# Optimization experiments

Hardware: AMD Instinct MI355X
Metric: run time of the kernel (lower is better)

## Reference

```python
import jax, jax.numpy as jnp
import numpy as np

B, S, D = 16, 2048, 512

def setup_inputs() -> dict:
    key = jax.random.key(0)
    k0, k1, k2, k3 = jax.random.split(key, 4)
    scale = 1.0 / np.sqrt(D)
    return {
        "inputs": jax.random.normal(k0, (B, S, D), dtype=jnp.float32),
        "W_q": jax.random.normal(k1, (D, D), dtype=jnp.float32) * scale,
        "W_k": jax.random.normal(k2, (D, D), dtype=jnp.float32) * scale,
        "W_v": jax.random.normal(k3, (D, D), dtype=jnp.float32) * scale,
    }

def reference(inputs, W_q, W_k, W_v):
    # Q/K/V projections: [B,S,D]
    q = jnp.einsum('bsd,de->bse', inputs, W_q)
    k = jnp.einsum('bsd,de->bse', inputs, W_k)
    v = jnp.einsum('bsd,de->bse', inputs, W_v)
    d_k = jnp.asarray(q.shape[-1], dtype=q.dtype)
    scores = jnp.einsum('bqd,bkd->bqk', q, k) / jnp.sqrt(d_k)  # [B,S,S]
    attn = jax.nn.softmax(scores, axis=-1)
    out = jnp.einsum('bqk,bkd->bqd', attn, v)  # [B,S,D]
    return jnp.sum(out, axis=1)  # sum-pool over seq -> [B,D]
```

## Files before the change

kernel.cpp:

```cpp
#include <hip/hip_runtime.h>
#include <hip/hip_bf16.h>


#define S_LEN 2048
#define D_DIM 512
#define BATCH 16

typedef short bf16x8 __attribute__((ext_vector_type(8)));
typedef float f32x4 __attribute__((ext_vector_type(4)));

typedef __attribute__((address_space(3))) void lds_void_t;
typedef const __attribute__((address_space(1))) void gbl_void_t;

__device__ __forceinline__ void async_copy16(const void* g, void* l) {
  __builtin_amdgcn_global_load_lds((gbl_void_t*)g, (lds_void_t*)l, 16, 0, 0);
}

__device__ __forceinline__ unsigned short f2bf(float f) {
  unsigned u = __float_as_uint(f);
  u += 0x7fff + ((u >> 16) & 1);
  return (unsigned short)(u >> 16);
}
__device__ __forceinline__ float bf2f(unsigned short h) {
  return __uint_as_float((unsigned)h << 16);
}

__device__ __forceinline__ unsigned enc8(float x) {
  unsigned u = __float_as_uint(x);
  unsigned t = (u + 0x7FFFFu + ((u >> 20) & 1u)) >> 20;
  int b = (int)t - 0x3C0;
  b = b < 0 ? 0 : (b > 127 ? 127 : b);
  return (unsigned)b;
}
__device__ __forceinline__ float dec8(unsigned b) {
  return b ? __uint_as_float((b + 0x3C0u) << 20) : 0.0f;
}

__device__ __forceinline__ void gemm_core_nt(
    const unsigned short* __restrict__ A, long lda,
    const unsigned short* __restrict__ B, long ldb,
    int K, unsigned short* As, unsigned short* Bs, f32x4 acc[4][4])
{
  const int tid  = threadIdx.x;
  const int lane = tid & 63;
  const int w    = tid >> 6;
  const int wm   = w >> 1, wn = w & 1;
  const int r16  = lane & 15;
  const int kq   = lane >> 4;

  const int j0 = w * 64 + lane;
  const int j1 = (w + 4) * 64 + lane;
  const int r0 = j0 >> 2, cc0 = (((j0 & 3) - (r0 >> 1)) & 3);
  const int r1 = j1 >> 2, cc1 = (((j1 & 3) - (r1 >> 1)) & 3);

  const long a0 = (long)r0 * lda + cc0 * 8;
  const long a1 = (long)r1 * lda + cc1 * 8;
  const long b0 = (long)r0 * ldb + cc0 * 8;
  const long b1 = (long)r1 * ldb + cc1 * 8;

  int aoff[4], boff[4];
#pragma unroll
  for (int mt = 0; mt < 4; ++mt) {
    const int row = wm * 64 + mt * 16 + r16;
    aoff[mt] = row * 32 + (((row >> 1) + kq) & 3) * 8;
  }
#pragma unroll
  for (int nt = 0; nt < 4; ++nt) {
    const int row = wn * 64 + nt * 16 + r16;
    boff[nt] = row * 32 + (((row >> 1) + kq) & 3) * 8;
  }

  for (int k0 = 0; k0 < K; k0 += 32) {
    __syncthreads();
    async_copy16(A + a0 + k0, (char*)As + (w    ) * 1024);
    async_copy16(A + a1 + k0, (char*)As + (w + 4) * 1024);
    async_copy16(B + b0 + k0, (char*)Bs + (w    ) * 1024);
    async_copy16(B + b1 + k0, (char*)Bs + (w + 4) * 1024);
    __syncthreads();

    bf16x8 af[4], bg[4];
#pragma unroll
    for (int mt = 0; mt < 4; ++mt) af[mt] = *(const bf16x8*)&As[aoff[mt]];
#pragma unroll
    for (int nt = 0; nt < 4; ++nt) bg[nt] = *(const bf16x8*)&Bs[boff[nt]];
#pragma unroll
    for (int mt = 0; mt < 4; ++mt)
#pragma unroll
      for (int nt = 0; nt < 4; ++nt)
        acc[mt][nt] = __builtin_amdgcn_mfma_f32_16x16x32_bf16(af[mt], bg[nt], acc[mt][nt], 0, 0, 0);
  }
}

__global__ __launch_bounds__(256) void k_zero(float* __restrict__ p, int n) {
  int i = blockIdx.x * 256 + threadIdx.x;
  if (i < n) p[i] = 0.0f;
}

__global__ __launch_bounds__(256) void k_cast(const float* __restrict__ s, unsigned short* __restrict__ d) {
  int i = (blockIdx.x * 256 + threadIdx.x) * 4;
  float4 v = *(const float4*)(s + i);
  ushort4 o;
  o.x = f2bf(v.x); o.y = f2bf(v.y); o.z = f2bf(v.z); o.w = f2bf(v.w);
  *(ushort4*)(d + i) = o;
}

__global__ __launch_bounds__(256) void k_castW(
    const float* __restrict__ a, const float* __restrict__ b,
    unsigned short* __restrict__ da, unsigned short* __restrict__ db)
{
  const int blk = blockIdx.x;
  const float* s = (blk < 256) ? a : b;
  unsigned short* d = (blk < 256) ? da : db;
  int i = ((blk & 255) * 256 + threadIdx.x) * 4;
  float4 v = *(const float4*)(s + i);
  ushort4 o;
  o.x = f2bf(v.x); o.y = f2bf(v.y); o.z = f2bf(v.z); o.w = f2bf(v.w);
  *(ushort4*)(d + i) = o;
}

__global__ __launch_bounds__(256) void k_gemm_bf16out(
    const unsigned short* __restrict__ A, long lda,
    const unsigned short* __restrict__ B, long ldb, int K,
    unsigned short* __restrict__ C, long ldc, float scale)
{
  __shared__ alignas(16) unsigned short As[128 * 32];
  __shared__ alignas(16) unsigned short Bs[128 * 32];
  f32x4 acc[4][4] = {};
  const long am0 = (long)blockIdx.y * 128;
  const long bn0 = (long)blockIdx.x * 128;
  gemm_core_nt(A + am0 * lda, lda, B + bn0 * ldb, ldb, K, As, Bs, acc);

  const int lane = threadIdx.x & 63;
  const int w = threadIdx.x >> 6, wm = w >> 1, wn = w & 1;
  const long row0 = am0 + wm * 64 + (lane >> 4) * 4;
  const long col0 = bn0 + wn * 64 + (lane & 15);
#pragma unroll
  for (int mt = 0; mt < 4; ++mt)
#pragma unroll
    for (int nt = 0; nt < 4; ++nt)
#pragma unroll
      for (int r = 0; r < 4; ++r)
        C[(row0 + mt * 16 + r) * ldc + col0 + nt * 16] = f2bf(acc[mt][nt][r] * scale);
}

union SMemAE {
  struct { unsigned short As[128 * 32]; unsigned short Bs[128 * 32]; } s;
  unsigned E32[128 * 36];
};

__global__ __launch_bounds__(256) void k_passAE(
    const unsigned short* __restrict__ Ybf, const unsigned short* __restrict__ Xbf,
    float* __restrict__ lrow, unsigned* __restrict__ E)
{
  __shared__ SMemAE sm;
  f32x4 acc[4][4] = {};
  const int b = blockIdx.z, qt = blockIdx.y, kt = blockIdx.x;
  const long q0 = (long)qt * 128;
  const long n0 = (long)kt * 128;
  gemm_core_nt(Ybf + ((long)b * S_LEN + q0) * D_DIM, D_DIM,
               Xbf + ((long)b * S_LEN + n0) * D_DIM, D_DIM, D_DIM,
               sm.s.As, sm.s.Bs, acc);

  const int lane = threadIdx.x & 63;
  const int w = threadIdx.x >> 6, wm = w >> 1, wn = w & 1;
  const int r16 = lane & 15, quad = lane >> 4;

  __syncthreads();

#pragma unroll
  for (int mt = 0; mt < 4; ++mt) {
    float rs[4] = {0.f, 0.f, 0.f, 0.f};
#pragma unroll
    for (int nt = 0; nt < 4; ++nt) {
      unsigned dw = 0;
#pragma unroll
      for (int r = 0; r < 4; ++r) {
        float e = __builtin_amdgcn_exp2f(acc[mt][nt][r]);
        rs[r] += e;
        dw |= enc8(e) << (8 * r);
      }
      const int col = wn * 64 + nt * 16 + r16;
      const int r4  = wm * 16 + mt * 4 + quad;
      sm.E32[col * 36 + r4] = dw;
    }
#pragma unroll
    for (int r = 0; r < 4; ++r) {
      float s = rs[r];
      s += __shfl_xor(s, 1, 64);
      s += __shfl_xor(s, 2, 64);
      s += __shfl_xor(s, 4, 64);
      s += __shfl_xor(s, 8, 64);
      if (r16 == 0)
        atomicAdd(&lrow[(long)b * S_LEN + q0 + wm * 64 + mt * 16 + quad * 4 + r], s);
    }
  }
  __syncthreads();

  unsigned* Eg = E + (((long)(b * 16 + qt)) * 16 + kt) * 4096;
  const int t = threadIdx.x;
#pragma unroll
  for (int p = 0; p < 4; ++p) {
    const int n = p * 256 + t;
    const int col = n >> 3, hj = n & 7;
    uint4 v = *(const uint4*)&sm.E32[col * 36 + hj * 4];
    *(uint4*)(Eg + n * 4) = v;
  }
}

__global__ __launch_bounds__(256) void k_wsum(
    const unsigned* __restrict__ E, const float* __restrict__ lrow,
    float* __restrict__ wcol)
{
  __shared__ float rl[512];
  const int kt = blockIdx.x, qq = blockIdx.y, b = blockIdx.z;
  const int tid = threadIdx.x;
  {
    const float* lp = lrow + (long)b * S_LEN + qq * 512;
    rl[tid]       = 1.0f / lp[tid];
    rl[tid + 256] = 1.0f / lp[tid + 256];
  }
  __syncthreads();
  const int col = tid & 127, qsel = tid >> 7;
  float acc = 0.0f;
#pragma unroll
  for (int qt2 = 0; qt2 < 2; ++qt2) {
    const int qtl = qsel * 2 + qt2;
    const int qt = qq * 4 + qtl;
    const unsigned* Ep = E + (((long)(b * 16 + qt)) * 16 + kt) * 4096 + col * 32;
    const float* rlq = rl + qtl * 128;
#pragma unroll
    for (int j = 0; j < 8; ++j) {
      uint4 v = *(const uint4*)(Ep + j * 4);
      const unsigned dws[4] = {v.x, v.y, v.z, v.w};
#pragma unroll
      for (int i = 0; i < 4; ++i) {
        const unsigned dv = dws[i];
        const float* r = rlq + j * 16 + i * 4;
        acc += dec8( dv        & 0xFFu) * r[0];
        acc += dec8((dv >>  8) & 0xFFu) * r[1];
        acc += dec8((dv >> 16) & 0xFFu) * r[2];
        acc += dec8((dv >> 24)        ) * r[3];
      }
    }
  }
  atomicAdd(&wcol[(long)b * S_LEN + kt * 128 + col], acc);
}

__global__ __launch_bounds__(256) void k_passA(
    const unsigned short* __restrict__ Ybf, const unsigned short* __restrict__ Xbf,
    float* __restrict__ lrow)
{
  __shared__ alignas(16) unsigned short As[128 * 32];
  __shared__ alignas(16) unsigned short Bs[128 * 32];
  f32x4 acc[4][4] = {};
  const int b = blockIdx.z;
  const long q0 = (long)blockIdx.y * 128;
  const long n0 = (long)blockIdx.x * 128;
  gemm_core_nt(Ybf + ((long)b * S_LEN + q0) * D_DIM, D_DIM,
               Xbf + ((long)b * S_LEN + n0) * D_DIM, D_DIM, D_DIM, As, Bs, acc);

  const int lane = threadIdx.x & 63;
  const int w = threadIdx.x >> 6, wm = w >> 1;
#pragma unroll
  for (int mt = 0; mt < 4; ++mt) {
#pragma unroll
    for (int r = 0; r < 4; ++r) {
      float s = 0.0f;
#pragma unroll
      for (int nt = 0; nt < 4; ++nt) s += __builtin_amdgcn_exp2f(acc[mt][nt][r]);
      s += __shfl_xor(s, 1, 64);
      s += __shfl_xor(s, 2, 64);
      s += __shfl_xor(s, 4, 64);
      s += __shfl_xor(s, 8, 64);
      if ((lane & 15) == 0)
        atomicAdd(&lrow[(long)b * S_LEN + q0 + wm * 64 + mt * 16 + (lane >> 4) * 4 + r], s);
    }
  }
}

__global__ __launch_bounds__(256) void k_passB(
    const unsigned short* __restrict__ Ybf, const unsigned short* __restrict__ Xbf,
    const float* __restrict__ lrow, float* __restrict__ wcol)
{
  __shared__ alignas(16) unsigned short As[128 * 32];
  __shared__ alignas(16) unsigned short Bs[128 * 32];
  f32x4 acc[4][4] = {};
  const int b = blockIdx.z;
  const long q0 = (long)blockIdx.y * 128;
  const long n0 = (long)blockIdx.x * 128;
  gemm_core_nt(Ybf + ((long)b * S_LEN + q0) * D_DIM, D_DIM,
               Xbf + ((long)b * S_LEN + n0) * D_DIM, D_DIM, D_DIM, As, Bs, acc);

  const int lane = threadIdx.x & 63;
  const int w = threadIdx.x >> 6, wm = w >> 1, wn = w & 1;
  float csv[4] = {0.0f, 0.0f, 0.0f, 0.0f};
#pragma unroll
  for (int mt = 0; mt < 4; ++mt) {
    const float4 lv = *(const float4*)&lrow[(long)b * S_LEN + q0 + wm * 64 + mt * 16 + (lane >> 4) * 4];
    const float rv[4] = {1.0f / lv.x, 1.0f / lv.y, 1.0f / lv.z, 1.0f / lv.w};
#pragma unroll
    for (int nt = 0; nt < 4; ++nt)
#pragma unroll
      for (int r = 0; r < 4; ++r)
        csv[nt] += __builtin_amdgcn_exp2f(acc[mt][nt][r]) * rv[r];
  }
#pragma unroll
  for (int nt = 0; nt < 4; ++nt) {
    csv[nt] += __shfl_xor(csv[nt], 16, 64);
    csv[nt] += __shfl_xor(csv[nt], 32, 64);
  }
  if (lane < 16) {
#pragma unroll
    for (int nt = 0; nt < 4; ++nt)
      atomicAdd(&wcol[(long)b * S_LEN + n0 + wn * 64 + nt * 16 + lane], csv[nt]);
  }
}

__global__ __launch_bounds__(256) void k_t(
    const unsigned short* __restrict__ Xbf, const float* __restrict__ wcol,
    float* __restrict__ tvec)
{
  const int b = blockIdx.z;
  const int d = blockIdx.x * 256 + threadIdx.x;
  const int k0 = blockIdx.y * 256;
  const unsigned short* Xp = Xbf + ((long)b * S_LEN + k0) * D_DIM + d;
  const float* wp = wcol + (long)b * S_LEN + k0;
  float acc = 0.0f;
#pragma unroll 4
  for (int k = 0; k < 256; ++k) acc += wp[k] * bf2f(Xp[(long)k * D_DIM]);
  atomicAdd(&tvec[b * D_DIM + d], acc);
}

__global__ __launch_bounds__(128) void k_out(
    const float* __restrict__ tvec, const float* __restrict__ Wv, float* __restrict__ out)
{
  __shared__ float tl[512];
  const int b = blockIdx.y;
  const int e = blockIdx.x * 128 + threadIdx.x;
#pragma unroll
  for (int j = 0; j < 4; ++j) tl[threadIdx.x + j * 128] = tvec[b * D_DIM + threadIdx.x + j * 128];
  __syncthreads();
  float acc = 0.0f;
#pragma unroll 4
  for (int d = 0; d < 512; ++d) acc += tl[d] * Wv[(long)d * D_DIM + e];
  out[b * D_DIM + e] = acc;
}

extern "C" void kernel_launch(void* const* d_in, const int* in_sizes, int n_in,
                              void* d_out, int out_size, void* d_ws, size_t ws_size,
                              hipStream_t stream) {
  const float* X  = (const float*)d_in[0];
  const float* Wq = (const float*)d_in[1];
  const float* Wk = (const float*)d_in[2];
  const float* Wv = (const float*)d_in[3];
  float* out = (float*)d_out;

  char* ws = (char*)d_ws;
  unsigned short* Xbf = (unsigned short*)(ws);
  unsigned short* Ybf = (unsigned short*)(ws + 33554432);
  unsigned short* Mt  = (unsigned short*)(ws + 67108864);
  unsigned short* Wqb = (unsigned short*)(ws + 67633152);
  unsigned short* Wkb = (unsigned short*)(ws + 68157440);
  float* lrow = (float*)(ws + 68681728);
  float* wcol = (float*)(ws + 68812800);
  float* tvec = (float*)(ws + 68943872);
  unsigned* E = (unsigned*)(ws + 69206016);
  const bool bigws = ws_size >= (size_t)69206016 + (size_t)67108864;

  k_zero<<<288, 256, 0, stream>>>(lrow, 73728);

  k_cast<<<16384, 256, 0, stream>>>(X, Xbf);
  k_castW<<<512, 256, 0, stream>>>(Wq, Wk, Wqb, Wkb);

  const float scale = 1.4426950408889634f / 22.627416997969522f;
  k_gemm_bf16out<<<dim3(4, 4), 256, 0, stream>>>(Wkb, 512, Wqb, 512, 512, Mt, 512, scale);

  k_gemm_bf16out<<<dim3(4, 256), 256, 0, stream>>>(Xbf, 512, Mt, 512, 512, Ybf, 512, 1.0f);

  if (bigws) {
    k_passAE<<<dim3(16, 16, 16), 256, 0, stream>>>(Ybf, Xbf, lrow, E);
    k_wsum<<<dim3(16, 4, 16), 256, 0, stream>>>(E, lrow, wcol);
  } else {
    k_passA<<<dim3(16, 16, 16), 256, 0, stream>>>(Ybf, Xbf, lrow);
    k_passB<<<dim3(16, 16, 16), 256, 0, stream>>>(Ybf, Xbf, lrow, wcol);
  }

  k_t<<<dim3(2, 8, 16), 256, 0, stream>>>(Xbf, wcol, tvec);
  k_out<<<dim3(4, 16), 128, 0, stream>>>(tvec, Wv, out);
}
```

Measured before the change: 324.1 us.

## Widen GEMM K-tile to 64, use hardware FP8 encode, split tail kernels

```diff
diff --git a/kernel.cpp b/kernel.cpp
--- a/kernel.cpp
+++ b/kernel.cpp
@@ -24,6 +24,12 @@
 __device__ __forceinline__ float bf2f(unsigned short h) {
   return __uint_as_float((unsigned)h << 16);
 }
+
+#if __has_builtin(__builtin_amdgcn_cvt_pk_fp8_f32) && __has_builtin(__builtin_amdgcn_cvt_f32_fp8)
+#define HAVE_FP8CVT 1
+#else
+#define HAVE_FP8CVT 0
+#endif
 
 __device__ __forceinline__ unsigned enc8(float x) {
   unsigned u = __float_as_uint(x);
@@ -36,6 +42,16 @@
   return b ? __uint_as_float((b + 0x3C0u) << 20) : 0.0f;
 }
 
+__device__ __forceinline__ unsigned pack4_fp8(float e0, float e1, float e2, float e3) {
+#if HAVE_FP8CVT
+  unsigned dw = (unsigned)__builtin_amdgcn_cvt_pk_fp8_f32(e0, e1, 0, false);
+  dw = (unsigned)__builtin_amdgcn_cvt_pk_fp8_f32(e2, e3, (int)dw, true);
+  return dw;
+#else
+  return enc8(e0) | (enc8(e1) << 8) | (enc8(e2) << 16) | (enc8(e3) << 24);
+#endif
+}
+
 __device__ __forceinline__ void gemm_core_nt(
     const unsigned short* __restrict__ A, long lda,
     const unsigned short* __restrict__ B, long ldb,
@@ -48,52 +64,58 @@
   const int r16  = lane & 15;
   const int kq   = lane >> 4;
 
-  const int j0 = w * 64 + lane;
-  const int j1 = (w + 4) * 64 + lane;
-  const int r0 = j0 >> 2, cc0 = (((j0 & 3) - (r0 >> 1)) & 3);
-  const int r1 = j1 >> 2, cc1 = (((j1 & 3) - (r1 >> 1)) & 3);
-
-  const long a0 = (long)r0 * lda + cc0 * 8;
-  const long a1 = (long)r1 * lda + cc1 * 8;
-  const long b0 = (long)r0 * ldb + cc0 * 8;
-  const long b1 = (long)r1 * ldb + cc1 * 8;
-
-  int aoff[4], boff[4];
-#pragma unroll
-  for (int mt = 0; mt < 4; ++mt) {
-    const int row = wm * 64 + mt * 16 + r16;
-    aoff[mt] = row * 32 + (((row >> 1) + kq) & 3) * 8;
-  }
-#pragma unroll
-  for (int nt = 0; nt < 4; ++nt) {
-    const int row = wn * 64 + nt * 16 + r16;
-    boff[nt] = row * 32 + (((row >> 1) + kq) & 3) * 8;
-  }
-
-  for (int k0 = 0; k0 < K; k0 += 32) {
+  long asrc[4], bsrc[4];
+#pragma unroll
+  for (int p = 0; p < 4; ++p) {
+    const int j = p * 256 + w * 64 + lane;
+    const int r = j >> 3, s = j & 7, c = (s - r) & 7;
+    asrc[p] = (long)r * lda + c * 8;
+    bsrc[p] = (long)r * ldb + c * 8;
+  }
+
+  int aoff[2][4], boff[2][4];
+#pragma unroll
+  for (int ks = 0; ks < 2; ++ks) {
+#pragma unroll
+    for (int t = 0; t < 4; ++t) {
+      const int m = wm * 64 + t * 16 + r16;
+      aoff[ks][t] = m * 64 + ((ks * 4 + kq + m) & 7) * 8;
+      const int n = wn * 64 + t * 16 + r16;
+      boff[ks][t] = n * 64 + ((ks * 4 + kq + n) & 7) * 8;
+    }
+  }
+
+  for (int k0 = 0; k0 < K; k0 += 64) {
     __syncthreads();
-    async_copy16(A + a0 + k0, (char*)As + (w    ) * 1024);
-    async_copy16(A + a1 + k0, (char*)As + (w + 4) * 1024);
-    async_copy16(B + b0 + k0, (char*)Bs + (w    ) * 1024);
-    async_copy16(B + b1 + k0, (char*)Bs + (w + 4) * 1024);
+#pragma unroll
+    for (int p = 0; p < 4; ++p) {
+      async_copy16(A + asrc[p] + k0, (char*)As + (p * 256 + w * 64) * 16);
+      async_copy16(B + bsrc[p] + k0, (char*)Bs + (p * 256 + w * 64) * 16);
+    }
     __syncthreads();
 
-    bf16x8 af[4], bg[4];
-#pragma unroll
-    for (int mt = 0; mt < 4; ++mt) af[mt] = *(const bf16x8*)&As[aoff[mt]];
-#pragma unroll
-    for (int nt = 0; nt < 4; ++nt) bg[nt] = *(const bf16x8*)&Bs[boff[nt]];
-#pragma unroll
-    for (int mt = 0; mt < 4; ++mt)
-#pragma unroll
-      for (int nt = 0; nt < 4; ++nt)
-        acc[mt][nt] = __builtin_amdgcn_mfma_f32_16x16x32_bf16(af[mt], bg[nt], acc[mt][nt], 0, 0, 0);
-  }
-}
-
-__global__ __launch_bounds__(256) void k_zero(float* __restrict__ p, int n) {
+#pragma unroll
+    for (int ks = 0; ks < 2; ++ks) {
+      bf16x8 af[4], bg[4];
+#pragma unroll
+      for (int mt = 0; mt < 4; ++mt) af[mt] = *(const bf16x8*)&As[aoff[ks][mt]];
+#pragma unroll
+      for (int nt = 0; nt < 4; ++nt) bg[nt] = *(const bf16x8*)&Bs[boff[ks][nt]];
+#pragma unroll
+      for (int mt = 0; mt < 4; ++mt)
+#pragma unroll
+        for (int nt = 0; nt < 4; ++nt)
+          acc[mt][nt] = __builtin_amdgcn_mfma_f32_16x16x32_bf16(af[mt], bg[nt], acc[mt][nt], 0, 0, 0);
+    }
+  }
+}
+
+__global__ __launch_bounds__(256) void k_zero2(float* __restrict__ p1, int n1,
+                                               float* __restrict__ p2, int n2) {
   int i = blockIdx.x * 256 + threadIdx.x;
-  if (i < n) p[i] = 0.0f;
+  if (i < n1) p1[i] = 0.0f;
+  i -= n1;
+  if (i >= 0 && i < n2) p2[i] = 0.0f;
 }
 
 __global__ __launch_bounds__(256) void k_cast(const float* __restrict__ s, unsigned short* __restrict__ d) {
@@ -123,8 +145,8 @@
     const unsigned short* __restrict__ B, long ldb, int K,
     unsigned short* __restrict__ C, long ldc, float scale)
 {
-  __shared__ alignas(16) unsigned short As[128 * 32];
-  __shared__ alignas(16) unsigned short Bs[128 * 32];
+  __shared__ alignas(16) unsigned short As[128 * 64];
+  __shared__ alignas(16) unsigned short Bs[128 * 64];
   f32x4 acc[4][4] = {};
   const long am0 = (long)blockIdx.y * 128;
   const long bn0 = (long)blockIdx.x * 128;
@@ -143,8 +165,8 @@
         C[(row0 + mt * 16 + r) * ldc + col0 + nt * 16] = f2bf(acc[mt][nt][r] * scale);
 }
 
-union SMemAE {
-  struct { unsigned short As[128 * 32]; unsigned short Bs[128 * 32]; } s;
+union alignas(16) SMemAE {
+  struct { unsigned short As[128 * 64]; unsigned short Bs[128 * 64]; } s;
   unsigned E32[128 * 36];
 };
 
@@ -172,16 +194,15 @@
     float rs[4] = {0.f, 0.f, 0.f, 0.f};
 #pragma unroll
     for (int nt = 0; nt < 4; ++nt) {
-      unsigned dw = 0;
+      float ev[4];
 #pragma unroll
       for (int r = 0; r < 4; ++r) {
-        float e = __builtin_amdgcn_exp2f(acc[mt][nt][r]);
-        rs[r] += e;
-        dw |= enc8(e) << (8 * r);
+        ev[r] = __builtin_amdgcn_exp2f(acc[mt][nt][r]);
+        rs[r] += ev[r];
       }
       const int col = wn * 64 + nt * 16 + r16;
       const int r4  = wm * 16 + mt * 4 + quad;
-      sm.E32[col * 36 + r4] = dw;
+      sm.E32[col * 36 + r4] = pack4_fp8(ev[0], ev[1], ev[2], ev[3]);
     }
 #pragma unroll
     for (int r = 0; r < 4; ++r) {
@@ -236,10 +257,17 @@
       for (int i = 0; i < 4; ++i) {
         const unsigned dv = dws[i];
         const float* r = rlq + j * 16 + i * 4;
+#if HAVE_FP8CVT
+        acc += __builtin_amdgcn_cvt_f32_fp8((int)dv, 0) * r[0];
+        acc += __builtin_amdgcn_cvt_f32_fp8((int)dv, 1) * r[1];
+        acc += __builtin_amdgcn_cvt_f32_fp8((int)dv, 2) * r[2];
+        acc += __builtin_amdgcn_cvt_f32_fp8((int)dv, 3) * r[3];
+#else
         acc += dec8( dv        & 0xFFu) * r[0];
         acc += dec8((dv >>  8) & 0xFFu) * r[1];
         acc += dec8((dv >> 16) & 0xFFu) * r[2];
         acc += dec8((dv >> 24)        ) * r[3];
+#endif
       }
     }
   }
@@ -250,8 +278,8 @@
     const unsigned short* __restrict__ Ybf, const unsigned short* __restrict__ Xbf,
     float* __restrict__ lrow)
 {
-  __shared__ alignas(16) unsigned short As[128 * 32];
-  __shared__ alignas(16) unsigned short Bs[128 * 32];
+  __shared__ alignas(16) unsigned short As[128 * 64];
+  __shared__ alignas(16) unsigned short Bs[128 * 64];
   f32x4 acc[4][4] = {};
   const int b = blockIdx.z;
   const long q0 = (long)blockIdx.y * 128;
@@ -282,8 +310,8 @@
     const unsigned short* __restrict__ Ybf, const unsigned short* __restrict__ Xbf,
     const float* __restrict__ lrow, float* __restrict__ wcol)
 {
-  __shared__ alignas(16) unsigned short As[128 * 32];
-  __shared__ alignas(16) unsigned short Bs[128 * 32];
+  __shared__ alignas(16) unsigned short As[128 * 64];
+  __shared__ alignas(16) unsigned short Bs[128 * 64];
   f32x4 acc[4][4] = {};
   const int b = blockIdx.z;
   const long q0 = (long)blockIdx.y * 128;
@@ -322,28 +350,28 @@
 {
   const int b = blockIdx.z;
   const int d = blockIdx.x * 256 + threadIdx.x;
-  const int k0 = blockIdx.y * 256;
+  const int k0 = blockIdx.y * 64;
   const unsigned short* Xp = Xbf + ((long)b * S_LEN + k0) * D_DIM + d;
   const float* wp = wcol + (long)b * S_LEN + k0;
   float acc = 0.0f;
-#pragma unroll 4
-  for (int k = 0; k < 256; ++k) acc += wp[k] * bf2f(Xp[(long)k * D_DIM]);
+#pragma unroll 8
+  for (int k = 0; k < 64; ++k) acc += wp[k] * bf2f(Xp[(long)k * D_DIM]);
   atomicAdd(&tvec[b * D_DIM + d], acc);
 }
 
 __global__ __launch_bounds__(128) void k_out(
     const float* __restrict__ tvec, const float* __restrict__ Wv, float* __restrict__ out)
 {
-  __shared__ float tl[512];
+  __shared__ float tl[128];
   const int b = blockIdx.y;
+  const int d0 = blockIdx.z * 128;
   const int e = blockIdx.x * 128 + threadIdx.x;
-#pragma unroll
-  for (int j = 0; j < 4; ++j) tl[threadIdx.x + j * 128] = tvec[b * D_DIM + threadIdx.x + j * 128];
+  tl[threadIdx.x] = tvec[b * D_DIM + d0 + threadIdx.x];
   __syncthreads();
   float acc = 0.0f;
-#pragma unroll 4
-  for (int d = 0; d < 512; ++d) acc += tl[d] * Wv[(long)d * D_DIM + e];
-  out[b * D_DIM + e] = acc;
+#pragma unroll 8
+  for (int d = 0; d < 128; ++d) acc += tl[d] * Wv[(long)(d0 + d) * D_DIM + e];
+  atomicAdd(&out[b * D_DIM + e], acc);
 }
 
 extern "C" void kernel_launch(void* const* d_in, const int* in_sizes, int n_in,
@@ -367,7 +395,7 @@
   unsigned* E = (unsigned*)(ws + 69206016);
   const bool bigws = ws_size >= (size_t)69206016 + (size_t)67108864;
 
-  k_zero<<<288, 256, 0, stream>>>(lrow, 73728);
+  k_zero2<<<320, 256, 0, stream>>>(lrow, 73728, out, BATCH * D_DIM);
 
   k_cast<<<16384, 256, 0, stream>>>(X, Xbf);
   k_castW<<<512, 256, 0, stream>>>(Wq, Wk, Wqb, Wkb);
@@ -385,6 +413,6 @@
     k_passB<<<dim3(16, 16, 16), 256, 0, stream>>>(Ybf, Xbf, lrow, wcol);
   }
 
-  k_t<<<dim3(2, 8, 16), 256, 0, stream>>>(Xbf, wcol, tvec);
-  k_out<<<dim3(4, 16), 128, 0, stream>>>(tvec, Wv, out);
-}
+  k_t<<<dim3(2, 32, 16), 256, 0, stream>>>(Xbf, wcol, tvec);
+  k_out<<<dim3(4, 16, 4), 128, 0, stream>>>(tvec, Wv, out);
+}
```

Measured after the change: 301.2 us. 7.1% less time.

## Fuse prep kernels, use hardware FP8 converts, and split small GEMV kernels

Applied to the files above, without the earlier changes.

```diff
diff --git a/kernel.cpp b/kernel.cpp
--- a/kernel.cpp
+++ b/kernel.cpp
@@ -24,6 +24,12 @@
 __device__ __forceinline__ float bf2f(unsigned short h) {
   return __uint_as_float((unsigned)h << 16);
 }
+
+#if __has_builtin(__builtin_amdgcn_cvt_pk_fp8_f32) && __has_builtin(__builtin_amdgcn_cvt_f32_fp8)
+#define HAVE_FP8CVT 1
+#else
+#define HAVE_FP8CVT 0
+#endif
 
 __device__ __forceinline__ unsigned enc8(float x) {
   unsigned u = __float_as_uint(x);
@@ -34,6 +40,16 @@
 }
 __device__ __forceinline__ float dec8(unsigned b) {
   return b ? __uint_as_float((b + 0x3C0u) << 20) : 0.0f;
+}
+
+__device__ __forceinline__ unsigned pack4_fp8(float e0, float e1, float e2, float e3) {
+#if HAVE_FP8CVT
+  unsigned dw = (unsigned)__builtin_amdgcn_cvt_pk_fp8_f32(e0, e1, 0, false);
+  dw = (unsigned)__builtin_amdgcn_cvt_pk_fp8_f32(e2, e3, (int)dw, true);
+  return dw;
+#else
+  return enc8(e0) | (enc8(e1) << 8) | (enc8(e2) << 16) | (enc8(e3) << 24);
+#endif
 }
 
 __device__ __forceinline__ void gemm_core_nt(
@@ -91,31 +107,82 @@
   }
 }
 
-__global__ __launch_bounds__(256) void k_zero(float* __restrict__ p, int n) {
-  int i = blockIdx.x * 256 + threadIdx.x;
-  if (i < n) p[i] = 0.0f;
-}
-
-__global__ __launch_bounds__(256) void k_cast(const float* __restrict__ s, unsigned short* __restrict__ d) {
-  int i = (blockIdx.x * 256 + threadIdx.x) * 4;
-  float4 v = *(const float4*)(s + i);
-  ushort4 o;
-  o.x = f2bf(v.x); o.y = f2bf(v.y); o.z = f2bf(v.z); o.w = f2bf(v.w);
-  *(ushort4*)(d + i) = o;
-}
-
-__global__ __launch_bounds__(256) void k_castW(
-    const float* __restrict__ a, const float* __restrict__ b,
-    unsigned short* __restrict__ da, unsigned short* __restrict__ db)
+__global__ __launch_bounds__(256) void k_prep(
+    const float* __restrict__ X, const float* __restrict__ Wq, const float* __restrict__ Wk,
+    unsigned short* __restrict__ Xbf, unsigned short* __restrict__ Wqb,
+    unsigned short* __restrict__ Wkb, float* __restrict__ zp, float* __restrict__ out)
 {
   const int blk = blockIdx.x;
-  const float* s = (blk < 256) ? a : b;
-  unsigned short* d = (blk < 256) ? da : db;
-  int i = ((blk & 255) * 256 + threadIdx.x) * 4;
-  float4 v = *(const float4*)(s + i);
-  ushort4 o;
-  o.x = f2bf(v.x); o.y = f2bf(v.y); o.z = f2bf(v.z); o.w = f2bf(v.w);
-  *(ushort4*)(d + i) = o;
+  if (blk < 16384) {
+    int i = (blk * 256 + threadIdx.x) * 4;
+    float4 v = *(const float4*)(X + i);
+    ushort4 o;
+    o.x = f2bf(v.x); o.y = f2bf(v.y); o.z = f2bf(v.z); o.w = f2bf(v.w);
+    *(ushort4*)(Xbf + i) = o;
+  } else if (blk < 16896) {
+    const int b2 = blk - 16384;
+    const float* s = (b2 < 256) ? Wq : Wk;
+    unsigned short* d = (b2 < 256) ? Wqb : Wkb;
+    int i = ((b2 & 255) * 256 + threadIdx.x) * 4;
+    float4 v = *(const float4*)(s + i);
+    ushort4 o;
+    o.x = f2bf(v.x); o.y = f2bf(v.y); o.z = f2bf(v.z); o.w = f2bf(v.w);
+    *(ushort4*)(d + i) = o;
+  } else {
+    int i = (blk - 16896) * 256 + threadIdx.x;
+    if (i < 73728) zp[i] = 0.0f;
+    else out[i - 73728] = 0.0f;
+  }
+}
+
+__global__ __launch_bounds__(256) void k_mt(
+    const unsigned short* __restrict__ A, const unsigned short* __restrict__ B,
+    unsigned short* __restrict__ C, float scale)
+{
+  __shared__ alignas(16) unsigned short As[64 * 32];
+  __shared__ alignas(16) unsigned short Bs[64 * 32];
+  f32x4 acc[2][2] = {};
+  const int tid = threadIdx.x, lane = tid & 63, w = tid >> 6;
+  const int wm = w >> 1, wn = w & 1, r16 = lane & 15, kq = lane >> 4;
+  const long a0row = (long)blockIdx.y * 64, b0row = (long)blockIdx.x * 64;
+
+  const int prow = tid >> 2, pslot = tid & 3, pc = (pslot - prow) & 3;
+  const long asrc = (a0row + prow) * 512 + pc * 8;
+  const long bsrc = (b0row + prow) * 512 + pc * 8;
+
+  int aoff[2], boff[2];
+#pragma unroll
+  for (int t = 0; t < 2; ++t) {
+    const int m = wm * 32 + t * 16 + r16;
+    aoff[t] = m * 32 + ((m + kq) & 3) * 8;
+    const int n = wn * 32 + t * 16 + r16;
+    boff[t] = n * 32 + ((n + kq) & 3) * 8;
+  }
+
+  for (int k0 = 0; k0 < 512; k0 += 32) {
+    __syncthreads();
+    async_copy16(A + asrc + k0, (char*)As + w * 1024);
+    async_copy16(B + bsrc + k0, (char*)Bs + w * 1024);
+    __syncthreads();
+    bf16x8 af[2], bg[2];
+#pragma unroll
+    for (int t = 0; t < 2; ++t) { af[t] = *(const bf16x8*)&As[aoff[t]]; bg[t] = *(const bf16x8*)&Bs[boff[t]]; }
+#pragma unroll
+    for (int mt = 0; mt < 2; ++mt)
+#pragma unroll
+      for (int nt = 0; nt < 2; ++nt)
+        acc[mt][nt] = __builtin_amdgcn_mfma_f32_16x16x32_bf16(af[mt], bg[nt], acc[mt][nt], 0, 0, 0);
+  }
+
+  const int quad = lane >> 4;
+#pragma unroll
+  for (int mt = 0; mt < 2; ++mt)
+#pragma unroll
+    for (int nt = 0; nt < 2; ++nt)
+#pragma unroll
+      for (int r = 0; r < 4; ++r)
+        C[(a0row + wm * 32 + mt * 16 + quad * 4 + r) * 512 + b0row + wn * 32 + nt * 16 + r16]
+            = f2bf(acc[mt][nt][r] * scale);
 }
 
 __global__ __launch_bounds__(256) void k_gemm_bf16out(
@@ -172,16 +239,15 @@
     float rs[4] = {0.f, 0.f, 0.f, 0.f};
 #pragma unroll
     for (int nt = 0; nt < 4; ++nt) {
-      unsigned dw = 0;
+      float ev[4];
 #pragma unroll
       for (int r = 0; r < 4; ++r) {
-        float e = __builtin_amdgcn_exp2f(acc[mt][nt][r]);
-        rs[r] += e;
-        dw |= enc8(e) << (8 * r);
+        ev[r] = __builtin_amdgcn_exp2f(acc[mt][nt][r]);
+        rs[r] += ev[r];
       }
       const int col = wn * 64 + nt * 16 + r16;
       const int r4  = wm * 16 + mt * 4 + quad;
-      sm.E32[col * 36 + r4] = dw;
+      sm.E32[col * 36 + r4] = pack4_fp8(ev[0], ev[1], ev[2], ev[3]);
     }
 #pragma unroll
     for (int r = 0; r < 4; ++r) {
@@ -236,10 +302,17 @@
       for (int i = 0; i < 4; ++i) {
         const unsigned dv = dws[i];
         const float* r = rlq + j * 16 + i * 4;
+#if HAVE_FP8CVT
+        acc += __builtin_amdgcn_cvt_f32_fp8((int)dv, 0) * r[0];
+        acc += __builtin_amdgcn_cvt_f32_fp8((int)dv, 1) * r[1];
+        acc += __builtin_amdgcn_cvt_f32_fp8((int)dv, 2) * r[2];
+        acc += __builtin_amdgcn_cvt_f32_fp8((int)dv, 3) * r[3];
+#else
         acc += dec8( dv        & 0xFFu) * r[0];
         acc += dec8((dv >>  8) & 0xFFu) * r[1];
         acc += dec8((dv >> 16) & 0xFFu) * r[2];
         acc += dec8((dv >> 24)        ) * r[3];
+#endif
       }
     }
   }
@@ -322,28 +395,28 @@
 {
   const int b = blockIdx.z;
   const int d = blockIdx.x * 256 + threadIdx.x;
-  const int k0 = blockIdx.y * 256;
+  const int k0 = blockIdx.y * 64;
   const unsigned short* Xp = Xbf + ((long)b * S_LEN + k0) * D_DIM + d;
   const float* wp = wcol + (long)b * S_LEN + k0;
   float acc = 0.0f;
-#pragma unroll 4
-  for (int k = 0; k < 256; ++k) acc += wp[k] * bf2f(Xp[(long)k * D_DIM]);
+#pragma unroll 8
+  for (int k = 0; k < 64; ++k) acc += wp[k] * bf2f(Xp[(long)k * D_DIM]);
   atomicAdd(&tvec[b * D_DIM + d], acc);
 }
 
 __global__ __launch_bounds__(128) void k_out(
     const float* __restrict__ tvec, const float* __restrict__ Wv, float* __restrict__ out)
 {
-  __shared__ float tl[512];
+  __shared__ float tl[128];
   const int b = blockIdx.y;
+  const int d0 = blockIdx.z * 128;
   const int e = blockIdx.x * 128 + threadIdx.x;
-#pragma unroll
-  for (int j = 0; j < 4; ++j) tl[threadIdx.x + j * 128] = tvec[b * D_DIM + threadIdx.x + j * 128];
+  tl[threadIdx.x] = tvec[b * D_DIM + d0 + threadIdx.x];
   __syncthreads();
   float acc = 0.0f;
-#pragma unroll 4
-  for (int d = 0; d < 512; ++d) acc += tl[d] * Wv[(long)d * D_DIM + e];
-  out[b * D_DIM + e] = acc;
+#pragma unroll 8
+  for (int d = 0; d < 128; ++d) acc += tl[d] * Wv[(long)(d0 + d) * D_DIM + e];
+  atomicAdd(&out[b * D_DIM + e], acc);
 }
 
 extern "C" void kernel_launch(void* const* d_in, const int* in_sizes, int n_in,
@@ -367,13 +440,10 @@
   unsigned* E = (unsigned*)(ws + 69206016);
   const bool bigws = ws_size >= (size_t)69206016 + (size_t)67108864;
 
-  k_zero<<<288, 256, 0, stream>>>(lrow, 73728);
-
-  k_cast<<<16384, 256, 0, stream>>>(X, Xbf);
-  k_castW<<<512, 256, 0, stream>>>(Wq, Wk, Wqb, Wkb);
+  k_prep<<<17216, 256, 0, stream>>>(X, Wq, Wk, Xbf, Wqb, Wkb, lrow, out);
 
   const float scale = 1.4426950408889634f / 22.627416997969522f;
-  k_gemm_bf16out<<<dim3(4, 4), 256, 0, stream>>>(Wkb, 512, Wqb, 512, 512, Mt, 512, scale);
+  k_mt<<<dim3(8, 8), 256, 0, stream>>>(Wkb, Wqb, Mt, scale);
 
   k_gemm_bf16out<<<dim3(4, 256), 256, 0, stream>>>(Xbf, 512, Mt, 512, 512, Ybf, 512, 1.0f);
 
@@ -385,6 +455,6 @@
     k_passB<<<dim3(16, 16, 16), 256, 0, stream>>>(Ybf, Xbf, lrow, wcol);
   }
 
-  k_t<<<dim3(2, 8, 16), 256, 0, stream>>>(Xbf, wcol, tvec);
-  k_out<<<dim3(4, 16), 128, 0, stream>>>(tvec, Wv, out);
-}
+  k_t<<<dim3(2, 32, 16), 256, 0, stream>>>(Xbf, wcol, tvec);
+  k_out<<<dim3(4, 16, 4), 128, 0, stream>>>(tvec, Wv, out);
+}
```

After: 272.3 us. 16.0% less time.
